# Kernel tuning notes

Measured on AMD Instinct MI355X. Metric: run time of the kernel, lower is better.

## Reference

```python
import jax, jax.numpy as jnp
import numpy as np

D = 768

def setup_inputs() -> dict:
    key = jax.random.key(0)
    k1, k2, k3, k4, k5 = jax.random.split(key, 5)
    query = jax.random.normal(k1, (32, 1024, D), dtype=jnp.float32)
    key_t = jax.random.normal(k2, (32, 1024, D), dtype=jnp.float32)
    w1 = jax.random.normal(k3, (1, D), dtype=jnp.float32) * 0.02
    w2 = jax.random.normal(k4, (1, D), dtype=jnp.float32) * 0.02
    w3 = jax.random.normal(k5, (1, D), dtype=jnp.float32) * 0.02
    return {"query": query, "key": key_t, "w1": w1, "w2": w2, "w3": w3}

def reference(query, key, w1, w2, w3):
    # q_logit: [B, Lq, 1], k_logit: [B, Lk, 1] -> transposed to [B, 1, Lk]
    q_logit = query @ w1[0]                       # [B, Lq]
    k_logit = key @ w2[0]                         # [B, Lk]
    dot_logit = jnp.einsum('bqd,bkd->bqk', query, w3[0] * key)  # [B, Lq, Lk]
    return q_logit[:, :, None] + k_logit[:, None, :] + dot_logit
```

## Files before the change

### kernel.cpp

```cpp
#include <hip/hip_runtime.h>
#include <hip/hip_bf16.h>

#define BB 32
#define LL 1024
#define DD 768

typedef short bf16x8 __attribute__((ext_vector_type(8)));
typedef float f32x4 __attribute__((ext_vector_type(4)));

__device__ __forceinline__ unsigned short f2bf(float f) {
    unsigned u = __builtin_bit_cast(unsigned, f);
    u += 0x7fffu + ((u >> 16) & 1u);
    return (unsigned short)(u >> 16);
}

__global__ __launch_bounds__(256) void convert_kernel(
    const float* __restrict__ Q, const float* __restrict__ K,
    const float* __restrict__ w1, const float* __restrict__ w2,
    const float* __restrict__ w3,
    unsigned short* __restrict__ Qb, unsigned short* __restrict__ Kb,
    float* __restrict__ qlog, float* __restrict__ klog)
{
    const int ln  = threadIdx.x & 63;
    const int row = blockIdx.x * 4 + (threadIdx.x >> 6);
    const size_t base = (size_t)row * DD;

    float qdot = 0.f, kdot = 0.f;
    #pragma unroll
    for (int c = 0; c < 3; ++c) {
        const int idx = c * 64 + ln;
        float4 qv  = ((const float4*)(Q + base))[idx];
        float4 kv  = ((const float4*)(K + base))[idx];
        float4 w1v = ((const float4*)w1)[idx];
        float4 w2v = ((const float4*)w2)[idx];
        float4 w3v = ((const float4*)w3)[idx];

        qdot += qv.x*w1v.x + qv.y*w1v.y + qv.z*w1v.z + qv.w*w1v.w;
        kdot += kv.x*w2v.x + kv.y*w2v.y + kv.z*w2v.z + kv.w*w2v.w;

        ushort4 pq, pk;
        pq.x = f2bf(qv.x); pq.y = f2bf(qv.y); pq.z = f2bf(qv.z); pq.w = f2bf(qv.w);
        pk.x = f2bf(kv.x * w3v.x); pk.y = f2bf(kv.y * w3v.y);
        pk.z = f2bf(kv.z * w3v.z); pk.w = f2bf(kv.w * w3v.w);
        ((ushort4*)(Qb + base))[idx] = pq;
        ((ushort4*)(Kb + base))[idx] = pk;
    }

    #pragma unroll
    for (int off = 32; off > 0; off >>= 1) {
        qdot += __shfl_down(qdot, off, 64);
        kdot += __shfl_down(kdot, off, 64);
    }
    if (ln == 0) { qlog[row] = qdot; klog[row] = kdot; }
}

__global__ __launch_bounds__(256) void trilinear_gemm(
    const unsigned short* __restrict__ Qb, const unsigned short* __restrict__ Kb,
    const float* __restrict__ qlog, const float* __restrict__ klog,
    float* __restrict__ out)
{
    __shared__ __align__(16) unsigned short As[3][128 * 32];
    __shared__ __align__(16) unsigned short Bs[3][128 * 32];

    const int tid  = threadIdx.x;
    const int w    = tid >> 6, lane = tid & 63;
    const int wq   = w >> 1, wk = w & 1;

    const int id = blockIdx.x;
    const int g  = id & 7;
    const int j  = id >> 3;
    const int b  = g + ((j >> 6) << 3);
    const int t0 = j & 63;
    const int qt = t0 >> 3, kt = t0 & 7;

    const unsigned short* Ag = Qb + ((size_t)b * LL + qt * 128) * DD;
    const unsigned short* Bg = Kb + ((size_t)b * LL + kt * 128) * DD;

    const int srow  = lane >> 2;
    const int scol  = ((lane & 3) ^ ((lane >> 3) & 3)) * 8;
    const int m    = lane & 15;
    const int l    = lane >> 4;
    const int p8   = (l ^ ((m >> 1) & 3)) * 8;

    f32x4 acc[4][4] = {};

    #define STAGE(kt_, s_) do {                                                  \
        const int k0_ = (kt_) * 32;                                              \
        _Pragma("unroll")                                                        \
        for (int j2 = 0; j2 < 2; ++j2) {                                         \
            const int rb_ = w * 32 + j2 * 16;         \
            __builtin_amdgcn_global_load_lds(                                    \
                (const __attribute__((address_space(1))) void*)                  \
                    (Ag + (size_t)(rb_ + srow) * DD + k0_ + scol),               \
                (__attribute__((address_space(3))) void*)&As[s_][rb_ * 32],      \
                16, 0, 0);                                                       \
            __builtin_amdgcn_global_load_lds(                                    \
                (const __attribute__((address_space(1))) void*)                  \
                    (Bg + (size_t)(rb_ + srow) * DD + k0_ + scol),               \
                (__attribute__((address_space(3))) void*)&Bs[s_][rb_ * 32],      \
                16, 0, 0);                                                       \
        }                                                                        \
    } while (0)

    #define COMPUTE(s_) do {                                                     \
        const unsigned short* A_ = As[s_];                                       \
        const unsigned short* B_ = Bs[s_];                                       \
        bf16x8 av[4], bv[4];                                                     \
        _Pragma("unroll")                                                        \
        for (int tt = 0; tt < 4; ++tt) {                                         \
            av[tt] = *(const bf16x8*)&A_[(wq * 64 + tt * 16 + m) * 32 + p8];     \
            bv[tt] = *(const bf16x8*)&B_[(wk * 64 + tt * 16 + m) * 32 + p8];     \
        }                                                                        \
        asm volatile("s_waitcnt lgkmcnt(0)" ::: "memory");                       \
        __builtin_amdgcn_sched_barrier(0);                                       \
        _Pragma("unroll")                                                        \
        for (int at = 0; at < 4; ++at)                                           \
            _Pragma("unroll")                                                    \
            for (int bt = 0; bt < 4; ++bt)                                       \
                acc[at][bt] = __builtin_amdgcn_mfma_f32_16x16x32_bf16(           \
                    av[at], bv[bt], acc[at][bt], 0, 0, 0);                       \
    } while (0)

    const int NT = DD / 32;

    STAGE(0, 0);
    STAGE(1, 1);
    asm volatile("s_waitcnt vmcnt(4)" ::: "memory");
    __builtin_amdgcn_s_barrier();
    __builtin_amdgcn_sched_barrier(0);

    int bc = 0, bs = 2;
    for (int t = 0; t < NT - 2; ++t) {
        STAGE(t + 2, bs);
        COMPUTE(bc);
        asm volatile("s_waitcnt vmcnt(4)" ::: "memory");
        __builtin_amdgcn_s_barrier();
        __builtin_amdgcn_sched_barrier(0);
        bc = (bc == 2) ? 0 : bc + 1;
        bs = (bs == 2) ? 0 : bs + 1;
    }
    COMPUTE(bc);
    asm volatile("s_waitcnt vmcnt(0)" ::: "memory");
    __builtin_amdgcn_s_barrier();
    __builtin_amdgcn_sched_barrier(0);
    bc = (bc == 2) ? 0 : bc + 1;
    COMPUTE(bc);

    #undef STAGE
    #undef COMPUTE

    const int qrow0 = qt * 128 + wq * 64;
    const int kcol0 = kt * 128 + wk * 64;
    const float* ql = qlog + b * LL + qrow0;
    const float* kl = klog + b * LL + kcol0;
    float* outp = out + ((size_t)b * LL + qrow0) * LL + kcol0;
    const int col = lane & 15, r4 = (lane >> 4) * 4;

    #pragma unroll
    for (int at = 0; at < 4; ++at) {
        #pragma unroll
        for (int bt = 0; bt < 4; ++bt) {
            const float klv = kl[bt * 16 + col];
            #pragma unroll
            for (int r = 0; r < 4; ++r) {
                const int row = at * 16 + r4 + r;
                outp[(size_t)row * LL + bt * 16 + col] = acc[at][bt][r] + ql[row] + klv;
            }
        }
    }
}

extern "C" void kernel_launch(void* const* d_in, const int* in_sizes, int n_in,
                              void* d_out, int out_size, void* d_ws, size_t ws_size,
                              hipStream_t stream) {
    const float* Q  = (const float*)d_in[0];
    const float* K  = (const float*)d_in[1];
    const float* w1 = (const float*)d_in[2];
    const float* w2 = (const float*)d_in[3];
    const float* w3 = (const float*)d_in[4];
    float* out = (float*)d_out;

    unsigned short* Qb = (unsigned short*)d_ws;
    unsigned short* Kb = Qb + (size_t)BB * LL * DD;
    float* qlog = (float*)(Kb + (size_t)BB * LL * DD);
    float* klog = qlog + BB * LL;

    convert_kernel<<<BB * LL / 4, 256, 0, stream>>>(Q, K, w1, w2, w3, Qb, Kb, qlog, klog);
    trilinear_gemm<<<2048, 256, 0, stream>>>(Qb, Kb, qlog, klog, out);
}
```

Measured before the change: 359.5 us.

## Enlarge GEMM tile to 256x256 with 8 waves and 4-stage pipeline

The batched GEMM block tile grows from 128x128 to 256x256, using 512 threads (8 waves, each computing 128x64) and a 4-deep LDS ring instead of 3. Larger tiles cut the global/L2 traffic per output element and keep more loads in flight. MFMA sections are wrapped in s_setprio, and the convert kernel stages the weight vectors in shared memory. In exchange the block uses 128 KB of LDS and twice the accumulator registers, and the grid shrinks to 512 blocks, which may reduce occupancy or cause spilling.

```diff
diff --git a/kernel.cpp b/kernel.cpp
--- a/kernel.cpp
+++ b/kernel.cpp
@@ -21,9 +21,25 @@
     unsigned short* __restrict__ Qb, unsigned short* __restrict__ Kb,
     float* __restrict__ qlog, float* __restrict__ klog)
 {
-    const int ln  = threadIdx.x & 63;
-    const int row = blockIdx.x * 4 + (threadIdx.x >> 6);
+    __shared__ __align__(16) float wsh[3 * DD];
+    const int tid = threadIdx.x;
+    #pragma unroll
+    for (int r = 0; r < 3; ++r) {
+        const int i = tid + r * 256;
+        if (i < 576) {
+            float4 v;
+            if      (i < 192) v = ((const float4*)w1)[i];
+            else if (i < 384) v = ((const float4*)w2)[i - 192];
+            else              v = ((const float4*)w3)[i - 384];
+            ((float4*)wsh)[i] = v;
+        }
+    }
+    __syncthreads();
+
+    const int ln  = tid & 63;
+    const int row = blockIdx.x * 4 + (tid >> 6);
     const size_t base = (size_t)row * DD;
+    const float4* wv = (const float4*)wsh;
 
     float qdot = 0.f, kdot = 0.f;
     #pragma unroll
@@ -31,9 +47,9 @@
         const int idx = c * 64 + ln;
         float4 qv  = ((const float4*)(Q + base))[idx];
         float4 kv  = ((const float4*)(K + base))[idx];
-        float4 w1v = ((const float4*)w1)[idx];
-        float4 w2v = ((const float4*)w2)[idx];
-        float4 w3v = ((const float4*)w3)[idx];
+        float4 w1v = wv[idx];
+        float4 w2v = wv[192 + idx];
+        float4 w3v = wv[384 + idx];
 
         qdot += qv.x*w1v.x + qv.y*w1v.y + qv.z*w1v.z + qv.w*w1v.w;
         kdot += kv.x*w2v.x + kv.y*w2v.y + kv.z*w2v.z + kv.w*w2v.w;
@@ -54,27 +70,27 @@
     if (ln == 0) { qlog[row] = qdot; klog[row] = kdot; }
 }
 
-__global__ __launch_bounds__(256) void trilinear_gemm(
+__global__ __launch_bounds__(512, 2) void trilinear_gemm(
     const unsigned short* __restrict__ Qb, const unsigned short* __restrict__ Kb,
     const float* __restrict__ qlog, const float* __restrict__ klog,
     float* __restrict__ out)
 {
-    __shared__ __align__(16) unsigned short As[3][128 * 32];
-    __shared__ __align__(16) unsigned short Bs[3][128 * 32];
+    __shared__ __align__(16) unsigned short As[4][256 * 32];
+    __shared__ __align__(16) unsigned short Bs[4][256 * 32];
 
     const int tid  = threadIdx.x;
     const int w    = tid >> 6, lane = tid & 63;
-    const int wq   = w >> 1, wk = w & 1;
+    const int wq   = w >> 2, wk = w & 3;
 
     const int id = blockIdx.x;
     const int g  = id & 7;
     const int j  = id >> 3;
-    const int b  = g + ((j >> 6) << 3);
-    const int t0 = j & 63;
-    const int qt = t0 >> 3, kt = t0 & 7;
-
-    const unsigned short* Ag = Qb + ((size_t)b * LL + qt * 128) * DD;
-    const unsigned short* Bg = Kb + ((size_t)b * LL + kt * 128) * DD;
+    const int b  = g + ((j >> 4) << 3);
+    const int t0 = j & 15;
+    const int qt = t0 >> 2, kt = t0 & 3;
+
+    const unsigned short* Ag = Qb + ((size_t)b * LL + qt * 256) * DD;
+    const unsigned short* Bg = Kb + ((size_t)b * LL + kt * 256) * DD;
 
     const int srow  = lane >> 2;
     const int scol  = ((lane & 3) ^ ((lane >> 3) & 3)) * 8;
@@ -82,13 +98,13 @@
     const int l    = lane >> 4;
     const int p8   = (l ^ ((m >> 1) & 3)) * 8;
 
-    f32x4 acc[4][4] = {};
+    f32x4 acc[8][4] = {};
 
     #define STAGE(kt_, s_) do {                                                  \
         const int k0_ = (kt_) * 32;                                              \
         _Pragma("unroll")                                                        \
         for (int j2 = 0; j2 < 2; ++j2) {                                         \
-            const int rb_ = w * 32 + j2 * 16;         \
+            const int rb_ = j2 * 128 + w * 16;        \
             __builtin_amdgcn_global_load_lds(                                    \
                 (const __attribute__((address_space(1))) void*)                  \
                     (Ag + (size_t)(rb_ + srow) * DD + k0_ + scol),               \
@@ -105,59 +121,68 @@
     #define COMPUTE(s_) do {                                                     \
         const unsigned short* A_ = As[s_];                                       \
         const unsigned short* B_ = Bs[s_];                                       \
-        bf16x8 av[4], bv[4];                                                     \
-        _Pragma("unroll")                                                        \
-        for (int tt = 0; tt < 4; ++tt) {                                         \
-            av[tt] = *(const bf16x8*)&A_[(wq * 64 + tt * 16 + m) * 32 + p8];     \
+        bf16x8 av[8], bv[4];                                                     \
+        _Pragma("unroll")                                                        \
+        for (int tt = 0; tt < 8; ++tt)                                           \
+            av[tt] = *(const bf16x8*)&A_[(wq * 128 + tt * 16 + m) * 32 + p8];    \
+        _Pragma("unroll")                                                        \
+        for (int tt = 0; tt < 4; ++tt)                                           \
             bv[tt] = *(const bf16x8*)&B_[(wk * 64 + tt * 16 + m) * 32 + p8];     \
-        }                                                                        \
         asm volatile("s_waitcnt lgkmcnt(0)" ::: "memory");                       \
         __builtin_amdgcn_sched_barrier(0);                                       \
-        _Pragma("unroll")                                                        \
-        for (int at = 0; at < 4; ++at)                                           \
+        __builtin_amdgcn_s_setprio(1);                                           \
+        _Pragma("unroll")                                                        \
+        for (int at = 0; at < 8; ++at)                                           \
             _Pragma("unroll")                                                    \
             for (int bt = 0; bt < 4; ++bt)                                       \
                 acc[at][bt] = __builtin_amdgcn_mfma_f32_16x16x32_bf16(           \
                     av[at], bv[bt], acc[at][bt], 0, 0, 0);                       \
+        __builtin_amdgcn_s_setprio(0);                                           \
     } while (0)
 
     const int NT = DD / 32;
 
     STAGE(0, 0);
     STAGE(1, 1);
+    STAGE(2, 2);
+    asm volatile("s_waitcnt vmcnt(8)" ::: "memory");
+    __builtin_amdgcn_s_barrier();
+    __builtin_amdgcn_sched_barrier(0);
+
+    int bc = 0, bs = 3;
+    for (int t = 0; t < NT - 3; ++t) {
+        STAGE(t + 3, bs);
+        COMPUTE(bc);
+        asm volatile("s_waitcnt vmcnt(8)" ::: "memory");
+        __builtin_amdgcn_s_barrier();
+        __builtin_amdgcn_sched_barrier(0);
+        bc = (bc + 1) & 3;
+        bs = (bs + 1) & 3;
+    }
+    COMPUTE(bc);
     asm volatile("s_waitcnt vmcnt(4)" ::: "memory");
     __builtin_amdgcn_s_barrier();
     __builtin_amdgcn_sched_barrier(0);
-
-    int bc = 0, bs = 2;
-    for (int t = 0; t < NT - 2; ++t) {
-        STAGE(t + 2, bs);
-        COMPUTE(bc);
-        asm volatile("s_waitcnt vmcnt(4)" ::: "memory");
-        __builtin_amdgcn_s_barrier();
-        __builtin_amdgcn_sched_barrier(0);
-        bc = (bc == 2) ? 0 : bc + 1;
-        bs = (bs == 2) ? 0 : bs + 1;
-    }
+    bc = (bc + 1) & 3;
     COMPUTE(bc);
     asm volatile("s_waitcnt vmcnt(0)" ::: "memory");
     __builtin_amdgcn_s_barrier();
     __builtin_amdgcn_sched_barrier(0);
-    bc = (bc == 2) ? 0 : bc + 1;
+    bc = (bc + 1) & 3;
     COMPUTE(bc);
 
     #undef STAGE
     #undef COMPUTE
 
-    const int qrow0 = qt * 128 + wq * 64;
-    const int kcol0 = kt * 128 + wk * 64;
+    const int qrow0 = qt * 256 + wq * 128;
+    const int kcol0 = kt * 256 + wk * 64;
     const float* ql = qlog + b * LL + qrow0;
     const float* kl = klog + b * LL + kcol0;
     float* outp = out + ((size_t)b * LL + qrow0) * LL + kcol0;
     const int col = lane & 15, r4 = (lane >> 4) * 4;
 
     #pragma unroll
-    for (int at = 0; at < 4; ++at) {
+    for (int at = 0; at < 8; ++at) {
         #pragma unroll
         for (int bt = 0; bt < 4; ++bt) {
             const float klv = kl[bt * 16 + col];
@@ -186,5 +211,5 @@
     float* klog = qlog + BB * LL;
 
     convert_kernel<<<BB * LL / 4, 256, 0, stream>>>(Q, K, w1, w2, w3, Qb, Kb, qlog, klog);
-    trilinear_gemm<<<2048, 256, 0, stream>>>(Qb, Kb, qlog, klog, out);
-}
+    trilinear_gemm<<<512, 512, 0, stream>>>(Qb, Kb, qlog, klog, out);
+}
```

New measurement: 360.4 us. No clear change (+0.3%).
